# Kernel optimization log

Hardware: AMD Instinct MI355X
Metric: run time of the kernel (lower is better)

The kernel has to match this reference:

```python
import jax, jax.numpy as jnp
import numpy as np

B, S, H = 4, 2048, 1024   # batch, seq_len, hidden_dim
E, D = 8, 1024            # num_experts, expert_dim (== hidden per module structure)
TOP_K = 2


def setup_inputs() -> dict:
    key = jax.random.key(0)
    ks = jax.random.split(key, 8)
    scale_h = 1.0 / np.sqrt(H)
    scale_d = 1.0 / np.sqrt(D)
    return {
        "x": jax.random.normal(ks[0], (B, S, H), dtype=jnp.float32),
        # router linear: hidden -> num_experts
        "w_router": jax.random.normal(ks[1], (H, E), dtype=jnp.float32) * scale_h,
        "b_router": jnp.zeros((E,), dtype=jnp.float32),
        # per-expert linear: hidden -> expert_dim
        "w_experts": jax.random.normal(ks[2], (E, H, D), dtype=jnp.float32) * scale_h,
        "b_experts": jnp.zeros((E, D), dtype=jnp.float32),
        # output linear: expert_dim -> expert_dim
        "w_out": jax.random.normal(ks[3], (D, D), dtype=jnp.float32) * scale_d,
        "b_out": jnp.zeros((D,), dtype=jnp.float32),
    }


def reference(x, w_router, b_router, w_experts, b_experts, w_out, b_out):
    # --- MoERouter: softmax over expert logits, top-2, renormalize ---
    logits = jnp.einsum("bsh,he->bse", x, w_router) + b_router          # [B,S,E]
    probs = jax.nn.softmax(logits, axis=-1)
    top_p, top_i = jax.lax.top_k(probs, TOP_K)                           # [B,S,2]
    top_p = top_p / jnp.sum(top_p, axis=-1, keepdims=True)
    # --- Dense expert compute over all tokens (module computes every expert) ---
    expert_out = jnp.einsum("bsh,ehd->bsed", x, w_experts) + b_experts   # [B,S,E,D]
    expert_out = jax.nn.gelu(expert_out)
    # --- Gather top-2 expert outputs and combine with routing weights ---
    sel = jnp.take_along_axis(expert_out, top_i[..., None], axis=2)      # [B,S,2,D]
    combined = jnp.sum(sel * top_p[..., None], axis=2)                   # [B,S,D]
    # --- Output projection ---
    return jnp.einsum("bsd,de->bse", combined, w_out) + b_out
```

## Files before the change

### kernel.cpp

```cpp
#include <hip/hip_runtime.h>


#define TOKENS 8192
#define HDIM   1024
#define DDIM   1024
#define NEXP   8

typedef __bf16 bf16x8 __attribute__((ext_vector_type(8)));
typedef float  f32x4  __attribute__((ext_vector_type(4)));

__device__ __forceinline__ unsigned short f2b(float f) {
  unsigned int u = __builtin_bit_cast(unsigned int, f);
  u = u + 0x7fffu + ((u >> 16) & 1u);
  return (unsigned short)(u >> 16);
}
__device__ __forceinline__ float b2f(unsigned short b) {
  unsigned int u = ((unsigned int)b) << 16;
  return __builtin_bit_cast(float, u);
}

__device__ __forceinline__ void gld_lds16(const void* g, void* l) {
  __builtin_amdgcn_global_load_lds(
      (__attribute__((address_space(1))) void*)(g),
      (__attribute__((address_space(3))) void*)(l),
      16, 0, 0);
}


__global__ void transpose_cvt_kernel(const float* __restrict__ we, const float* __restrict__ wo,
                                     unsigned short* __restrict__ weT, unsigned short* __restrict__ woT) {
  __shared__ unsigned short tile[32][33];
  int z = blockIdx.z;
  const float* s;
  unsigned short* d;
  if (z < 8) { s = we + (size_t)z * HDIM * DDIM; d = weT + (size_t)z * HDIM * DDIM; }
  else       { s = wo;                            d = woT; }
  int bx = blockIdx.x * 32;
  int by = blockIdx.y * 32;
  for (int i = threadIdx.y; i < 32; i += 8)
    tile[i][threadIdx.x] = f2b(s[(size_t)(by + i) * 1024 + bx + threadIdx.x]);
  __syncthreads();
  for (int i = threadIdx.y; i < 32; i += 8)
    d[(size_t)(bx + i) * 1024 + by + threadIdx.x] = tile[threadIdx.x][i];
}


__global__ void router_compute_kernel(const float* __restrict__ x, const float* __restrict__ wr,
                                      const float* __restrict__ br,
                                      int* __restrict__ eidx, float* __restrict__ ew,
                                      unsigned short* __restrict__ xb) {
  int wave = threadIdx.x >> 6, lane = threadIdx.x & 63;
  int t = blockIdx.x * 4 + wave;
  const float* xp = x + (size_t)t * HDIM;
  unsigned short* xbp = xb + (size_t)t * HDIM;
  float acc[8];
#pragma unroll
  for (int e = 0; e < 8; ++e) acc[e] = 0.f;
#pragma unroll
  for (int h0 = 0; h0 < HDIM; h0 += 256) {
    int h = h0 + lane * 4;
    float4 xv = *(const float4*)&xp[h];
    ushort4 o;
    o.x = f2b(xv.x); o.y = f2b(xv.y); o.z = f2b(xv.z); o.w = f2b(xv.w);
    *(ushort4*)&xbp[h] = o;
    float xq[4] = {xv.x, xv.y, xv.z, xv.w};
#pragma unroll
    for (int q = 0; q < 4; ++q) {
      const float4* wp = (const float4*)&wr[(h + q) * 8];
      float4 w0 = wp[0], w1 = wp[1];
      acc[0] += xq[q] * w0.x; acc[1] += xq[q] * w0.y; acc[2] += xq[q] * w0.z; acc[3] += xq[q] * w0.w;
      acc[4] += xq[q] * w1.x; acc[5] += xq[q] * w1.y; acc[6] += xq[q] * w1.z; acc[7] += xq[q] * w1.w;
    }
  }
#pragma unroll
  for (int off = 32; off; off >>= 1)
#pragma unroll
    for (int e = 0; e < 8; ++e) acc[e] += __shfl_xor(acc[e], off, 64);
  if (lane == 0) {
    float l[8], p[8];
    float m = -1e30f;
#pragma unroll
    for (int e = 0; e < 8; ++e) { l[e] = acc[e] + br[e]; m = fmaxf(m, l[e]); }
    float s = 0.f;
#pragma unroll
    for (int e = 0; e < 8; ++e) { p[e] = __expf(l[e] - m); s += p[e]; }
    int i1 = 0;
#pragma unroll
    for (int e = 1; e < 8; ++e) if (p[e] > p[i1]) i1 = e;
    int i2 = (i1 == 0) ? 1 : 0;
#pragma unroll
    for (int e = 0; e < 8; ++e) if (e != i1 && p[e] > p[i2]) i2 = e;
    float ps = p[i1] + p[i2];
    eidx[t * 2]     = i1;  ew[t * 2]     = p[i1] / ps;
    eidx[t * 2 + 1] = i2;  ew[t * 2 + 1] = p[i2] / ps;
  }
}


__global__ __launch_bounds__(1024) void build_lists_kernel(
    const int* __restrict__ eidx, const float* ew,
    int* __restrict__ counts, int* __restrict__ tok2, float* __restrict__ wl,
    int* s2p) {
  int e = blockIdx.x;
  int tid = threadIdx.x;
  int lane = tid & 63, wv = tid >> 6;
  __shared__ int wsum[16];
  __shared__ int base;
  if (tid == 0) base = 0;
  __syncthreads();
  for (int c = 0; c < 2 * TOKENS; c += 1024) {
    int i = c + tid;
    bool m = (eidx[i] == e);
    unsigned long long bal = __ballot(m);
    if (lane == 0) wsum[wv] = __popcll(bal);
    __syncthreads();
    int wbase = base;
    for (int w = 0; w < wv; ++w) wbase += wsum[w];
    if (m) {
      int pos = wbase + __popcll(bal & ((1ull << lane) - 1ull));
      float w = ew[i];
      tok2[e * TOKENS + pos] = i;
      wl[e * TOKENS + pos] = w;
      s2p[i] = pos;
    }
    int total = 0;
#pragma unroll
    for (int w = 0; w < 16; ++w) total += wsum[w];
    __syncthreads();
    if (tid == 0) base += total;
    __syncthreads();
  }
  if (tid == 0) counts[e] = base;
}


__global__ __launch_bounds__(256, 3) void expert_gemm_kernel(
    const unsigned short* __restrict__ xb, const unsigned short* __restrict__ weT,
    const float* __restrict__ b_experts, const int* __restrict__ counts,
    const int* __restrict__ tok2, const float* __restrict__ wlist,
    unsigned short* __restrict__ outE) {
  int b = blockIdx.x;
  int id = (b >> 3) + (b & 7) * 512;
  int e = id >> 9;
  int rem = id & 511;
  int m0 = (rem >> 3) << 7;
  int n0 = (rem & 7) << 7;
  int cnt = counts[e];
  if (m0 >= cnt) return;
  int cbase = 0;
  for (int q = 0; q < e; ++q) cbase += counts[q];

  __shared__ unsigned short As[3][128 * 32];
  __shared__ unsigned short Bs[3][128 * 32];
  __shared__ int   tokS[128];
  __shared__ float wS[128];

  int tid = threadIdx.x;
  if (tid < 128) {
    int r = m0 + tid;
    tokS[tid] = (r < cnt) ? tok2[e * TOKENS + r] : 0;
    wS[tid]   = (r < cnt) ? wlist[e * TOKENS + r] : 0.f;
  }
  __syncthreads();

  int wave = tid >> 6, lane = tid & 63;
  int subr = lane >> 2, koff = (lane & 3) * 8;

  const unsigned short* wbase = weT + (size_t)e * (HDIM * DDIM);
  const unsigned short* asrc[2];
  const unsigned short* bsrc[2];
  unsigned short* adst[3][2];
  unsigned short* bdst[3][2];
#pragma unroll
  for (int i = 0; i < 2; ++i) {
    int row = i * 64 + wave * 16 + subr;
    asrc[i] = xb + (size_t)(tokS[row] >> 1) * HDIM + koff;
    bsrc[i] = wbase + (size_t)(n0 + row) * HDIM + koff;
#pragma unroll
    for (int bb = 0; bb < 3; ++bb) {
      adst[bb][i] = &As[bb][i * 2048 + wave * 512];
      bdst[bb][i] = &Bs[bb][i * 2048 + wave * 512];
    }
  }

  int wm = wave & 1, wn = wave >> 1;
  int quad = lane >> 4, lr = lane & 15;

  f32x4 zero = {0.f, 0.f, 0.f, 0.f};
  f32x4 acc[4][4];
#pragma unroll
  for (int i = 0; i < 4; ++i)
#pragma unroll
    for (int j = 0; j < 4; ++j) acc[i][j] = zero;

#pragma unroll
  for (int s = 0; s < 2; ++s)
#pragma unroll
    for (int i = 0; i < 2; ++i) {
      gld_lds16(asrc[i] + s * 32, adst[s][i]);
      gld_lds16(bsrc[i] + s * 32, bdst[s][i]);
    }

#pragma unroll
  for (int kk = 0; kk < 32; ++kk) {
    if (kk < 31) asm volatile("s_waitcnt vmcnt(4)" ::: "memory");
    else         asm volatile("s_waitcnt vmcnt(0)" ::: "memory");
    __builtin_amdgcn_s_barrier();
    if (kk + 2 < 32) {
      int nb = (kk + 2) % 3;
      int off = (kk + 2) * 32;
#pragma unroll
      for (int i = 0; i < 2; ++i) {
        gld_lds16(asrc[i] + off, adst[nb][i]);
        gld_lds16(bsrc[i] + off, bdst[nb][i]);
      }
    }
    int cb = kk % 3;
    bf16x8 af[4], bfr[4];
#pragma unroll
    for (int i = 0; i < 4; ++i)
      af[i] = *(const bf16x8*)&As[cb][(wm * 64 + i * 16 + lr) * 32 + quad * 8];
#pragma unroll
    for (int j = 0; j < 4; ++j)
      bfr[j] = *(const bf16x8*)&Bs[cb][(wn * 64 + j * 16 + lr) * 32 + quad * 8];
#pragma unroll
    for (int i = 0; i < 4; ++i)
#pragma unroll
      for (int j = 0; j < 4; ++j)
        acc[i][j] = __builtin_amdgcn_mfma_f32_16x16x32_bf16(af[i], bfr[j], acc[i][j], 0, 0, 0);
  }

  int rowbase = cbase + m0;
#pragma unroll
  for (int j = 0; j < 4; ++j) {
    int col = n0 + wn * 64 + j * 16 + lr;
    float bias = b_experts[e * DDIM + col];
#pragma unroll
    for (int i = 0; i < 4; ++i) {
      int rbase = wm * 64 + i * 16 + quad * 4;
#pragma unroll
      for (int r = 0; r < 4; ++r) {
        int row = rbase + r;
        if (m0 + row < cnt) {
          float h = acc[i][j][r] + bias;
          float z = 0.7978845608f * (h + 0.044715f * h * h * h);
          float t = 1.f - 2.f / (__expf(2.f * z) + 1.f);
          float g = 0.5f * h * (1.f + t);
          outE[(size_t)(rowbase + row) * DDIM + col] = f2b(g * wS[row]);
        }
      }
    }
  }
}


__global__ void combine_kernel(const ushort4* __restrict__ outE,
                               const int* __restrict__ eidx, const int* __restrict__ s2p,
                               const int* __restrict__ counts,
                               ushort4* __restrict__ comb) {
  __shared__ int cbase[8];
  int tid = threadIdx.x;
  if (tid < 8) {
    int s = 0;
    for (int q = 0; q < tid; ++q) s += counts[q];
    cbase[tid] = s;
  }
  __syncthreads();
  int t = blockIdx.x;
  int d4 = tid;
  int i0 = t * 2, i1 = i0 + 1;
  size_t r0 = ((size_t)(cbase[eidx[i0]] + s2p[i0])) * 256 + d4;
  size_t r1 = ((size_t)(cbase[eidx[i1]] + s2p[i1])) * 256 + d4;
  ushort4 a = outE[r0];
  ushort4 b = outE[r1];
  ushort4 o;
  o.x = f2b(b2f(a.x) + b2f(b.x));
  o.y = f2b(b2f(a.y) + b2f(b.y));
  o.z = f2b(b2f(a.z) + b2f(b.z));
  o.w = f2b(b2f(a.w) + b2f(b.w));
  comb[t * 256 + d4] = o;
}


__global__ __launch_bounds__(256, 3) void out_gemm_kernel(
    const unsigned short* __restrict__ Abf, const unsigned short* __restrict__ BT,
    const float* __restrict__ bias, float* __restrict__ out) {
  int b = blockIdx.x;
  int id = (b >> 3) + (b & 7) * 64;
  int n0 = (id >> 6) << 7;
  int m0 = (id & 63) << 7;

  __shared__ unsigned short As[3][128 * 32];
  __shared__ unsigned short Bs[3][128 * 32];
  int tid = threadIdx.x, wave = tid >> 6, lane = tid & 63;
  int subr = lane >> 2, koff = (lane & 3) * 8;

  const unsigned short* asrc[2];
  const unsigned short* bsrc[2];
  unsigned short* adst[3][2];
  unsigned short* bdst[3][2];
#pragma unroll
  for (int i = 0; i < 2; ++i) {
    int row = i * 64 + wave * 16 + subr;
    asrc[i] = Abf + (size_t)(m0 + row) * DDIM + koff;
    bsrc[i] = BT + (size_t)(n0 + row) * DDIM + koff;
#pragma unroll
    for (int bb = 0; bb < 3; ++bb) {
      adst[bb][i] = &As[bb][i * 2048 + wave * 512];
      bdst[bb][i] = &Bs[bb][i * 2048 + wave * 512];
    }
  }

  int wm = wave & 1, wn = wave >> 1;
  int quad = lane >> 4, lr = lane & 15;

  f32x4 zero = {0.f, 0.f, 0.f, 0.f};
  f32x4 acc[4][4];
#pragma unroll
  for (int i = 0; i < 4; ++i)
#pragma unroll
    for (int j = 0; j < 4; ++j) acc[i][j] = zero;

#pragma unroll
  for (int s = 0; s < 2; ++s)
#pragma unroll
    for (int i = 0; i < 2; ++i) {
      gld_lds16(asrc[i] + s * 32, adst[s][i]);
      gld_lds16(bsrc[i] + s * 32, bdst[s][i]);
    }

#pragma unroll
  for (int kk = 0; kk < 32; ++kk) {
    if (kk < 31) asm volatile("s_waitcnt vmcnt(4)" ::: "memory");
    else         asm volatile("s_waitcnt vmcnt(0)" ::: "memory");
    __builtin_amdgcn_s_barrier();
    if (kk + 2 < 32) {
      int nb = (kk + 2) % 3;
      int off = (kk + 2) * 32;
#pragma unroll
      for (int i = 0; i < 2; ++i) {
        gld_lds16(asrc[i] + off, adst[nb][i]);
        gld_lds16(bsrc[i] + off, bdst[nb][i]);
      }
    }
    int cb = kk % 3;
    bf16x8 af[4], bfr[4];
#pragma unroll
    for (int i = 0; i < 4; ++i)
      af[i] = *(const bf16x8*)&As[cb][(wm * 64 + i * 16 + lr) * 32 + quad * 8];
#pragma unroll
    for (int j = 0; j < 4; ++j)
      bfr[j] = *(const bf16x8*)&Bs[cb][(wn * 64 + j * 16 + lr) * 32 + quad * 8];
#pragma unroll
    for (int i = 0; i < 4; ++i)
#pragma unroll
      for (int j = 0; j < 4; ++j)
        acc[i][j] = __builtin_amdgcn_mfma_f32_16x16x32_bf16(af[i], bfr[j], acc[i][j], 0, 0, 0);
  }

#pragma unroll
  for (int j = 0; j < 4; ++j) {
    int col = n0 + wn * 64 + j * 16 + lr;
    float bs = bias[col];
#pragma unroll
    for (int i = 0; i < 4; ++i) {
      int rbase = wm * 64 + i * 16 + quad * 4;
#pragma unroll
      for (int r = 0; r < 4; ++r)
        out[(size_t)(m0 + rbase + r) * DDIM + col] = acc[i][j][r] + bs;
    }
  }
}


extern "C" void kernel_launch(void* const* d_in, const int* in_sizes, int n_in,
                              void* d_out, int out_size, void* d_ws, size_t ws_size,
                              hipStream_t stream) {
  const float* x  = (const float*)d_in[0];
  const float* wr = (const float*)d_in[1];
  const float* br = (const float*)d_in[2];
  const float* we = (const float*)d_in[3];
  const float* be = (const float*)d_in[4];
  const float* wo = (const float*)d_in[5];
  const float* bo = (const float*)d_in[6];
  float* out = (float*)d_out;

  char* ws = (char*)d_ws;
  unsigned short* xb      = (unsigned short*)(ws);
  unsigned short* weT     = (unsigned short*)(ws + 16777216);
  unsigned short* woT     = (unsigned short*)(ws + 33554432);
  unsigned short* outE    = (unsigned short*)(ws + 35651584);
  int*            counts  = (int*)           (ws + 69206016);
  int*            tok2    = (int*)           (ws + 69206272);
  float*          wlist   = (float*)         (ws + 69468416);
  int*            eidx    = (int*)           (ws + 69730560);
  float*          ew      = (float*)         (ws + 69796096);
  int*            s2p     = (int*)ew;
  unsigned short* comb    = xb;

  router_compute_kernel<<<2048, 256, 0, stream>>>(x, wr, br, eidx, ew, xb);
  transpose_cvt_kernel<<<dim3(32, 32, 9), dim3(32, 8), 0, stream>>>(we, wo, weT, woT);
  build_lists_kernel<<<8, 1024, 0, stream>>>(eidx, ew, counts, tok2, wlist, s2p);
  expert_gemm_kernel<<<4096, 256, 0, stream>>>(xb, weT, be, counts, tok2, wlist, outE);
  combine_kernel<<<8192, 256, 0, stream>>>((const ushort4*)outE, eidx, s2p, counts, (ushort4*)comb);
  out_gemm_kernel<<<512, 256, 0, stream>>>(comb, woT, bo, out);
}
```

Measured before the change: 282.3 us.

## Merge router and weight-transpose kernels; load gathered A rows directly into registers

```diff
diff --git a/kernel.cpp b/kernel.cpp
--- a/kernel.cpp
+++ b/kernel.cpp
@@ -27,29 +27,34 @@
 }
 
 
-__global__ void transpose_cvt_kernel(const float* __restrict__ we, const float* __restrict__ wo,
-                                     unsigned short* __restrict__ weT, unsigned short* __restrict__ woT) {
+__global__ __launch_bounds__(256) void pre_kernel(
+    const float* __restrict__ x, const float* __restrict__ wr,
+    const float* __restrict__ br,
+    const float* __restrict__ we, const float* __restrict__ wo,
+    unsigned short* __restrict__ weT, unsigned short* __restrict__ woT,
+    unsigned short* __restrict__ xb,
+    int* __restrict__ eidx, float* __restrict__ ew) {
   __shared__ unsigned short tile[32][33];
-  int z = blockIdx.z;
-  const float* s;
-  unsigned short* d;
-  if (z < 8) { s = we + (size_t)z * HDIM * DDIM; d = weT + (size_t)z * HDIM * DDIM; }
-  else       { s = wo;                            d = woT; }
-  int bx = blockIdx.x * 32;
-  int by = blockIdx.y * 32;
-  for (int i = threadIdx.y; i < 32; i += 8)
-    tile[i][threadIdx.x] = f2b(s[(size_t)(by + i) * 1024 + bx + threadIdx.x]);
-  __syncthreads();
-  for (int i = threadIdx.y; i < 32; i += 8)
-    d[(size_t)(bx + i) * 1024 + by + threadIdx.x] = tile[threadIdx.x][i];
-}
-
-
-__global__ void router_compute_kernel(const float* __restrict__ x, const float* __restrict__ wr,
-                                      const float* __restrict__ br,
-                                      int* __restrict__ eidx, float* __restrict__ ew,
-                                      unsigned short* __restrict__ xb) {
-  int wave = threadIdx.x >> 6, lane = threadIdx.x & 63;
+  int tid = threadIdx.x;
+  if (blockIdx.x >= 2048) {
+    int lid = blockIdx.x - 2048;
+    int z = lid >> 10;
+    int rem = lid & 1023;
+    int bx = (rem & 31) * 32;
+    int by = (rem >> 5) * 32;
+    const float* s;
+    unsigned short* d;
+    if (z < 8) { s = we + (size_t)z * HDIM * DDIM; d = weT + (size_t)z * HDIM * DDIM; }
+    else       { s = wo;                            d = woT; }
+    int tx = tid & 31, ty = tid >> 5;
+    for (int i = ty; i < 32; i += 8)
+      tile[i][tx] = f2b(s[(size_t)(by + i) * 1024 + bx + tx]);
+    __syncthreads();
+    for (int i = ty; i < 32; i += 8)
+      d[(size_t)(bx + i) * 1024 + by + tx] = tile[tx][i];
+    return;
+  }
+  int wave = tid >> 6, lane = tid & 63;
   int t = blockIdx.x * 4 + wave;
   const float* xp = x + (size_t)t * HDIM;
   unsigned short* xbp = xb + (size_t)t * HDIM;
@@ -150,7 +155,6 @@
   int cbase = 0;
   for (int q = 0; q < e; ++q) cbase += counts[q];
 
-  __shared__ unsigned short As[3][128 * 32];
   __shared__ unsigned short Bs[3][128 * 32];
   __shared__ int   tokS[128];
   __shared__ float wS[128];
@@ -167,25 +171,25 @@
   int subr = lane >> 2, koff = (lane & 3) * 8;
 
   const unsigned short* wbase = weT + (size_t)e * (HDIM * DDIM);
-  const unsigned short* asrc[2];
   const unsigned short* bsrc[2];
-  unsigned short* adst[3][2];
   unsigned short* bdst[3][2];
 #pragma unroll
   for (int i = 0; i < 2; ++i) {
     int row = i * 64 + wave * 16 + subr;
-    asrc[i] = xb + (size_t)(tokS[row] >> 1) * HDIM + koff;
     bsrc[i] = wbase + (size_t)(n0 + row) * HDIM + koff;
 #pragma unroll
-    for (int bb = 0; bb < 3; ++bb) {
-      adst[bb][i] = &As[bb][i * 2048 + wave * 512];
+    for (int bb = 0; bb < 3; ++bb)
       bdst[bb][i] = &Bs[bb][i * 2048 + wave * 512];
-    }
   }
 
   int wm = wave & 1, wn = wave >> 1;
   int quad = lane >> 4, lr = lane & 15;
 
+  const unsigned short* aptr[4];
+#pragma unroll
+  for (int i = 0; i < 4; ++i)
+    aptr[i] = xb + (size_t)(tokS[wm * 64 + i * 16 + lr] >> 1) * HDIM + quad * 8;
+
   f32x4 zero = {0.f, 0.f, 0.f, 0.f};
   f32x4 acc[4][4];
 #pragma unroll
@@ -193,41 +197,40 @@
 #pragma unroll
     for (int j = 0; j < 4; ++j) acc[i][j] = zero;
 
-#pragma unroll
-  for (int s = 0; s < 2; ++s)
-#pragma unroll
-    for (int i = 0; i < 2; ++i) {
-      gld_lds16(asrc[i] + s * 32, adst[s][i]);
-      gld_lds16(bsrc[i] + s * 32, bdst[s][i]);
-    }
+  bf16x8 areg[2][4];
+#pragma unroll
+  for (int i = 0; i < 2; ++i) gld_lds16(bsrc[i], bdst[0][i]);
+  asm volatile("" ::: "memory");
+#pragma unroll
+  for (int i = 0; i < 4; ++i) areg[0][i] = *(const bf16x8*)(aptr[i]);
+  asm volatile("" ::: "memory");
+#pragma unroll
+  for (int i = 0; i < 2; ++i) gld_lds16(bsrc[i] + 32, bdst[1][i]);
 
 #pragma unroll
   for (int kk = 0; kk < 32; ++kk) {
-    if (kk < 31) asm volatile("s_waitcnt vmcnt(4)" ::: "memory");
-    else         asm volatile("s_waitcnt vmcnt(0)" ::: "memory");
+    if (kk < 31) asm volatile("s_waitcnt vmcnt(6)" ::: "memory");
+    else         asm volatile("s_waitcnt vmcnt(4)" ::: "memory");
     __builtin_amdgcn_s_barrier();
+    if (kk < 31) {
+#pragma unroll
+      for (int i = 0; i < 4; ++i)
+        areg[(kk + 1) & 1][i] = *(const bf16x8*)(aptr[i] + (kk + 1) * 32);
+    }
     if (kk + 2 < 32) {
-      int nb = (kk + 2) % 3;
-      int off = (kk + 2) * 32;
-#pragma unroll
-      for (int i = 0; i < 2; ++i) {
-        gld_lds16(asrc[i] + off, adst[nb][i]);
-        gld_lds16(bsrc[i] + off, bdst[nb][i]);
-      }
-    }
-    int cb = kk % 3;
-    bf16x8 af[4], bfr[4];
+#pragma unroll
+      for (int i = 0; i < 2; ++i)
+        gld_lds16(bsrc[i] + (kk + 2) * 32, bdst[(kk + 2) % 3][i]);
+    }
+    bf16x8 bfr[4];
+#pragma unroll
+    for (int j = 0; j < 4; ++j)
+      bfr[j] = *(const bf16x8*)&Bs[kk % 3][(wn * 64 + j * 16 + lr) * 32 + quad * 8];
 #pragma unroll
     for (int i = 0; i < 4; ++i)
-      af[i] = *(const bf16x8*)&As[cb][(wm * 64 + i * 16 + lr) * 32 + quad * 8];
-#pragma unroll
-    for (int j = 0; j < 4; ++j)
-      bfr[j] = *(const bf16x8*)&Bs[cb][(wn * 64 + j * 16 + lr) * 32 + quad * 8];
-#pragma unroll
-    for (int i = 0; i < 4; ++i)
 #pragma unroll
       for (int j = 0; j < 4; ++j)
-        acc[i][j] = __builtin_amdgcn_mfma_f32_16x16x32_bf16(af[i], bfr[j], acc[i][j], 0, 0, 0);
+        acc[i][j] = __builtin_amdgcn_mfma_f32_16x16x32_bf16(areg[kk & 1][i], bfr[j], acc[i][j], 0, 0, 0);
   }
 
   int rowbase = cbase + m0;
@@ -398,8 +401,8 @@
   int*            s2p     = (int*)ew;
   unsigned short* comb    = xb;
 
-  router_compute_kernel<<<2048, 256, 0, stream>>>(x, wr, br, eidx, ew, xb);
-  transpose_cvt_kernel<<<dim3(32, 32, 9), dim3(32, 8), 0, stream>>>(we, wo, weT, woT);
+  pre_kernel<<<2048 + 9216, 256, 0, stream>>>(x, wr, br, we, wo, weT, woT,
+                                              xb, eidx, ew);
   build_lists_kernel<<<8, 1024, 0, stream>>>(eidx, ew, counts, tok2, wlist, s2p);
   expert_gemm_kernel<<<4096, 256, 0, stream>>>(xb, weT, be, counts, tok2, wlist, outE);
   combine_kernel<<<8192, 256, 0, stream>>>((const ushort4*)outE, eidx, s2p, counts, (ushort4*)comb);
```

New measurement: 306.9 us. 8.7% more time.
